# Performance work log

Hardware: AMD Instinct MI355X
Metric: run time of the kernel (lower is better)

## Reference

```python
import jax, jax.numpy as jnp
import numpy as np

EMB_DIM = 256
NUM_EMB = 8192
COMMITMENT = 0.25
DECAY = 0.99
EPSILON = 1e-05


def setup_inputs() -> dict:
    key = jax.random.key(0)
    k1, k2, k3 = jax.random.split(key, 3)
    inputs = jax.random.normal(k1, (32, EMB_DIM, 32, 32), dtype=jnp.float32)
    embed = jax.random.normal(k2, (EMB_DIM, NUM_EMB), dtype=jnp.float32)
    cluster_size = jnp.ones((NUM_EMB,), dtype=jnp.float32)
    ema_embed = jax.random.normal(k3, (EMB_DIM, NUM_EMB), dtype=jnp.float32)
    return {"inputs": inputs, "embed": embed, "cluster_size": cluster_size, "ema_embed": ema_embed}


def reference(inputs, embed, cluster_size, ema_embed):
    # NCHW -> NHWC
    x = jnp.transpose(inputs, (0, 2, 3, 1))  # [B,H,W,D]
    in_shape = x.shape
    flatten = x.reshape(-1, EMB_DIM)  # [N,D]
    N = flatten.shape[0]

    dist = (jnp.sum(flatten ** 2, axis=1, keepdims=True)
            - 2.0 * flatten @ embed
            + jnp.sum(embed ** 2, axis=0, keepdims=True))
    idx = jnp.argmin(dist, axis=1)  # [N]

    # codebook gather
    quantize = embed.T[idx].reshape(in_shape)  # [B,H,W,D]

    # ---- EMA updates (training mode) ----
    counts = jnp.zeros((NUM_EMB,), flatten.dtype).at[idx].add(1.0)  # one-hot col sums
    new_cluster_size = cluster_size * DECAY + (1.0 - DECAY) * counts
    n = jnp.sum(new_cluster_size)
    smoothed = n * ((new_cluster_size + EPSILON) / (n + new_cluster_size * EPSILON))
    dw = jax.ops.segment_sum(flatten, idx, num_segments=NUM_EMB).T  # [D,K] == flatten.T @ onehot
    new_ema_embed = ema_embed * DECAY + (1.0 - DECAY) * dw
    new_embed = new_ema_embed / smoothed[None, :]

    # losses / straight-through
    e_latent_loss = jnp.mean((jax.lax.stop_gradient(quantize) - x) ** 2)
    loss = COMMITMENT * e_latent_loss
    quant_st = x + jax.lax.stop_gradient(quantize - x)

    avg_probs = counts / N
    perplexity = jnp.exp(-jnp.sum(avg_probs * jnp.log(avg_probs + 1e-10)))

    out = jnp.transpose(quant_st, (0, 3, 1, 2))  # back to NCHW
    return (out, loss, perplexity, new_cluster_size, new_embed, new_ema_embed)
```

## Files before the change

### kernel.cpp

```cpp
#include <hip/hip_runtime.h>
#include <math.h>


#define KC 8192
#define DD 256
#define NV 32768

typedef _Float16 f16;
typedef _Float16 f16x8 __attribute__((ext_vector_type(8)));
typedef _Float16 f16x4 __attribute__((ext_vector_type(4)));
typedef float f32x4 __attribute__((ext_vector_type(4)));
typedef unsigned int u32;
typedef unsigned long long u64;

#define DBIAS 4096.0f

__device__ __forceinline__ u32 umin32(u32 a, u32 b) { return a < b ? a : b; }
__device__ __forceinline__ u32 umax32(u32 a, u32 b) { return a > b ? a : b; }

__global__ __launch_bounds__(256, 2) void k_convert_x(
    const float* __restrict__ x, f16* __restrict__ xh, f16* __restrict__ xl,
    float* __restrict__ lossAcc) {
    __shared__ float xs[256][68];
    __shared__ float red[4];
    const int t = threadIdx.x;
    const int n0 = blockIdx.x * 64;
    const int b = n0 >> 10;
    const int h0 = (n0 >> 5) & 31;
    {
        const int p = t >> 7, tt = t & 127;
        const int wq = (tt & 7) * 4, d0 = tt >> 3;
        const float* src = x + (size_t)b * 262144 + (size_t)(h0 + p) * 32 + wq;
        float s2 = 0.f;
        #pragma unroll
        for (int i = 0; i < 16; ++i) {
            int d = d0 + i * 16;
            float4 v = *(const float4*)(src + (size_t)d * 1024);
            *(float4*)&xs[d][p * 32 + wq] = v;
            s2 += v.x * v.x + v.y * v.y + v.z * v.z + v.w * v.w;
        }
        for (int off = 32; off > 0; off >>= 1) s2 += __shfl_xor(s2, off);
        if ((t & 63) == 0) red[t >> 6] = s2;
    }
    __syncthreads();
    if (t == 0) atomicAdd(&lossAcc[1], red[0] + red[1] + red[2] + red[3]);
    {
        const int rr = t & 3, c = t >> 2;
        #pragma unroll
        for (int i = 0; i < 16; ++i) {
            int r = rr + i * 4;
            f16x4 hv, lv;
            #pragma unroll
            for (int q = 0; q < 4; ++q) {
                float v = xs[c * 4 + q][r];
                f16 h = (f16)v;
                float rem = v - (float)h;
                hv[q] = h; lv[q] = (f16)rem;
            }
            *(f16x4*)(xh + (size_t)(n0 + r) * DD + c * 4) = hv;
            *(f16x4*)(xl + (size_t)(n0 + r) * DD + c * 4) = lv;
        }
    }
}

__global__ __launch_bounds__(256, 2) void k_convert_e(
    const float* __restrict__ embed, f16* __restrict__ eh, f16* __restrict__ el,
    float* __restrict__ enorm, float* __restrict__ lossAcc) {
    __shared__ float ps2[8][33];
    __shared__ float psl[8][33];
    const int t = threadIdx.x;
    const int c = t & 31, g = t >> 5;
    const int k = blockIdx.x * 32 + c;
    const int d0 = g * 32;
    f16x8 hv[4], lv[4];
    float s2 = 0.f, sl2 = 0.f;
    #pragma unroll
    for (int i = 0; i < 32; ++i) {
        float v = embed[(size_t)(d0 + i) * KC + k];
        f16 h = (f16)v;
        float rem = v - (float)h;
        f16 lo = (f16)rem;
        hv[i >> 3][i & 7] = h;
        lv[i >> 3][i & 7] = lo;
        s2 += v * v;
        float lf = (float)lo;
        sl2 += lf * lf;
    }
    #pragma unroll
    for (int i = 0; i < 4; ++i) {
        *(f16x8*)(eh + (size_t)k * DD + d0 + i * 8) = hv[i];
        *(f16x8*)(el + (size_t)k * DD + d0 + i * 8) = lv[i];
    }
    ps2[g][c] = s2; psl[g][c] = sl2;
    __syncthreads();
    if (t < 32) {
        float e = 0.f, l = 0.f;
        #pragma unroll
        for (int g2 = 0; g2 < 8; ++g2) { e += ps2[g2][t]; l += psl[g2][t]; }
        enorm[blockIdx.x * 32 + t] = e;
        float me = e, mll = l;
        #pragma unroll
        for (int off = 16; off > 0; off >>= 1) {
            me = fmaxf(me, __shfl_xor(me, off));
            mll = fmaxf(mll, __shfl_xor(mll, off));
        }
        if (t == 0) {
            atomicMax((int*)(lossAcc + 2), __float_as_int(me));
            atomicMax((int*)(lossAcc + 3), __float_as_int(mll));
        }
    }
}


__device__ __forceinline__ void gload16(const void* g, void* l) {
    __builtin_amdgcn_global_load_lds(
        (const __attribute__((address_space(1))) void*)g,
        (__attribute__((address_space(3))) void*)l, 16, 0, 0);
}

#define CFENCE asm volatile("" ::: "memory")
#define BAR()  do { CFENCE; __builtin_amdgcn_s_barrier(); CFENCE; } while (0)
#define WAITV(N) asm volatile("s_waitcnt vmcnt(" #N ")" ::: "memory")
#define WAITL0   asm volatile("s_waitcnt lgkmcnt(0)" ::: "memory")

#define STAGE(KT, NB) do { \
    const f16* _ga = xh + aoff + (KT) * 32; \
    gload16(_ga, ldsAw + (NB) * 16384); \
    gload16(_ga + 16 * DD, ldsAw + (NB) * 16384 + 1024); \
    gload16(eh + boff + (KT) * 32, ldsBw + (NB) * 8192); \
} while (0)

#define PHASE(B, DOSTAGE, SKT, SNB, WN) do { \
    const char* _ab = AsB + (B) * 16384 + abyte; \
    const char* _bb = BsB + (B) * 8192 + bbyte; \
    f16x8 _aav[4], _bbv[4]; \
    _Pragma("unroll") for (int _j = 0; _j < 4; ++_j) _bbv[_j] = *(const f16x8*)(_bb + _j * 1024); \
    _Pragma("unroll") for (int _i = 0; _i < 4; ++_i) _aav[_i] = *(const f16x8*)(_ab + _i * 1024); \
    WAITL0; BAR(); \
    if (DOSTAGE) { STAGE(SKT, SNB); } \
    __builtin_amdgcn_s_setprio(1); \
    _Pragma("unroll") for (int _i = 0; _i < 4; ++_i) \
    _Pragma("unroll") for (int _j = 0; _j < 4; ++_j) \
        acc[_i][_j] = __builtin_amdgcn_mfma_f32_16x16x32_f16(_aav[_i], _bbv[_j], acc[_i][_j], 0, 0, 0); \
    __builtin_amdgcn_s_setprio(0); \
    asm volatile("s_waitcnt vmcnt(" #WN ")" ::: "memory"); BAR(); \
} while (0)

#define PFINAL(B) do { \
    const char* _ab = AsB + (B) * 16384 + abyte; \
    const char* _bb = BsB + (B) * 8192 + bbyte; \
    f16x8 _aav[4], _bbv[4]; \
    _Pragma("unroll") for (int _j = 0; _j < 4; ++_j) _bbv[_j] = *(const f16x8*)(_bb + _j * 1024); \
    _Pragma("unroll") for (int _i = 0; _i < 4; ++_i) _aav[_i] = *(const f16x8*)(_ab + _i * 1024); \
    WAITL0; \
    __builtin_amdgcn_s_setprio(1); \
    _Pragma("unroll") for (int _i = 0; _i < 4; ++_i) \
    _Pragma("unroll") for (int _j = 0; _j < 4; ++_j) \
        acc[_i][_j] = __builtin_amdgcn_mfma_f32_16x16x32_f16(_aav[_i], _bbv[_j], acc[_i][_j], 0, 0, 0); \
    __builtin_amdgcn_s_setprio(0); \
} while (0)

#define DPPSTEP(CTRL) do { \
    u32 _b0 = (u32)__builtin_amdgcn_update_dpp((int)a0v, (int)a0v, CTRL, 0xF, 0xF, false); \
    u32 _b1 = (u32)__builtin_amdgcn_update_dpp((int)a1v, (int)a1v, CTRL, 0xF, 0xF, false); \
    u32 _mx = umax32(a0v, _b0); \
    a0v = umin32(a0v, _b0); \
    a1v = umin32(_mx, umin32(a1v, _b1)); \
} while (0)

__global__ __launch_bounds__(512, 4) void k_gemm_cand(
    const f16* __restrict__ xh, const f16* __restrict__ eh,
    const float* __restrict__ enorm, u64* __restrict__ cand) {
    __shared__ f16 As[3][8192];
    __shared__ f16 Bs[3][4096];
    __shared__ float en_s[128];

    const int t = threadIdx.x;
    const int lane = t & 63, wid = t >> 6;
    const int wr = wid >> 1, wc = wid & 1;
    const int m = lane & 15, q = lane >> 4;

    const int bid = blockIdx.x;
    const int xcd = bid & 7, seq = bid >> 3;
    const int colb = seq >> 4;
    const int rowb = (xcd << 4) | (seq & 15);
    const int BR = rowb * 256;
    const int CBb = colb * 128;

    char* AsB = (char*)&As[0][0];
    char* BsB = (char*)&Bs[0][0];

    if (t < 128) en_s[t] = enorm[CBb + t] + DBIAS;

    const int u8 = lane >> 3, cx = (lane & 7) ^ u8;
    const int stg_row = 2 * u8 + (cx >> 2);
    const int stg_col = (cx & 3) * 8;
    const size_t aoff = (size_t)(BR + wid * 32 + stg_row) * DD + stg_col;
    const size_t boff = (size_t)(CBb + wid * 16 + stg_row) * DD + stg_col;
    char* const ldsAw = AsB + wid * 2048;
    char* const ldsBw = BsB + wid * 1024;

    const int rdsw = (((((m & 1) << 2) | q)) ^ (m >> 1)) * 16;
    const int abyte = wr * 4096 + (m >> 1) * 128 + rdsw;
    const int bbyte = wc * 4096 + (m >> 1) * 128 + rdsw;

    f32x4 acc[4][4];
    #pragma unroll
    for (int i = 0; i < 4; ++i)
        #pragma unroll
        for (int j = 0; j < 4; ++j) acc[i][j] = (f32x4){0.f, 0.f, 0.f, 0.f};

    STAGE(0, 0); STAGE(1, 1);
    WAITV(3); BAR();

    PHASE(0, 1, 2, 2, 3);
    PHASE(1, 1, 3, 0, 3);
    PHASE(2, 1, 4, 1, 3);
    PHASE(0, 1, 5, 2, 3);
    PHASE(1, 1, 6, 0, 3);
    PHASE(2, 1, 7, 1, 3);
    PHASE(0, 0, 0, 0, 0);
    PFINAL(1);

    const int sslab = colb * 2 + wc;
    float enb[4];
    #pragma unroll
    for (int j = 0; j < 4; ++j) enb[j] = en_s[wc * 64 + j * 16 + m];
    #pragma unroll
    for (int i = 0; i < 4; ++i)
    #pragma unroll
    for (int r = 0; r < 4; ++r) {
        u32 kk[4];
        #pragma unroll
        for (int j = 0; j < 4; ++j) {
            float dv = __builtin_fmaf(-2.f, acc[i][j][r], enb[j]);
            kk[j] = (__float_as_uint(dv) & 0xFFFFFFC0u) | (u32)(j * 16 + m);
        }
        u32 s1 = umin32(kk[0], kk[1]), g1 = umax32(kk[0], kk[1]);
        u32 s2 = umin32(kk[2], kk[3]), g2 = umax32(kk[2], kk[3]);
        u32 a0v = umin32(s1, s2);
        u32 a1v = umin32(umax32(s1, s2), umin32(g1, g2));
        DPPSTEP(0x111);
        DPPSTEP(0x112);
        DPPSTEP(0x114);
        DPPSTEP(0x118);
        if (m == 15) {
            int row = BR + wr * 64 + i * 16 + q * 4 + r;
            cand[(size_t)row * 128 + sslab] = ((u64)a1v << 32) | a0v;
        }
    }
}

__global__ __launch_bounds__(256) void k_rescore(
    const u64* __restrict__ cand, const f16* __restrict__ xh, const f16* __restrict__ xl,
    const f16* __restrict__ eh, const f16* __restrict__ el,
    const float* __restrict__ enorm, int* __restrict__ idx, int* __restrict__ cnt,
    float* __restrict__ lossAcc) {
    __shared__ float lred[4];
    const int t = threadIdx.x, l = t & 63, w = t >> 6;
    const int n = blockIdx.x * 4 + w;
    const int l4 = l * 4;

    u64 p0 = cand[(size_t)n * 128 + l];
    u64 p1 = cand[(size_t)n * 128 + 64 + l];
    u32 e0 = (u32)p0, e1 = (u32)(p0 >> 32), e2 = (u32)p1, e3 = (u32)(p1 >> 32);

    u32 mk = umin32(umin32(e0, e1), umin32(e2, e3));
    #pragma unroll
    for (int off = 1; off < 64; off <<= 1)
        mk = umin32(mk, (u32)__shfl_xor((int)mk, off));
    float gminb = __uint_as_float(mk & 0xFFFFFFC0u);

    f16x4 hv = *(const f16x4*)(xh + (size_t)n * DD + l4);
    f16x4 lv = *(const f16x4*)(xl + (size_t)n * DD + l4);
    float xf0 = (float)hv[0] + (float)lv[0];
    float xf1 = (float)hv[1] + (float)lv[1];
    float xf2 = (float)hv[2] + (float)lv[2];
    float xf3 = (float)hv[3] + (float)lv[3];
    float xh2 = (float)hv[0]*(float)hv[0] + (float)hv[1]*(float)hv[1]
              + (float)hv[2]*(float)hv[2] + (float)hv[3]*(float)hv[3];
    float xl2 = (float)lv[0]*(float)lv[0] + (float)lv[1]*(float)lv[1]
              + (float)lv[2]*(float)lv[2] + (float)lv[3]*(float)lv[3];
    #pragma unroll
    for (int off = 1; off < 64; off <<= 1) {
        xh2 += __shfl_xor(xh2, off);
        xl2 += __shfl_xor(xl2, off);
    }
    float maxE2 = lossAcc[2], maxEl2 = lossAcc[3];
    float dlt = 2.f * (sqrtf(xh2) * sqrtf(maxEl2) + sqrtf(xl2) * sqrtf(maxE2));
    float tau = gminb + 2.f * dlt * 1.02f + 0.2f;

    float best = 3.4e38f;
    int bestc = 1 << 30;

#define SLOT(ENT, SBASE) do { \
    float _av = __uint_as_float((ENT) & 0xFFFFFFC0u); \
    u64 _bm = __ballot(_av <= tau); \
    while (_bm) { \
        int _src = __ffsll((unsigned long long)_bm) - 1; _bm &= _bm - 1; \
        u32 _ee = (u32)__shfl((int)(ENT), _src); \
        int _code = ((SBASE) + _src) * 64 + (int)(_ee & 63u); \
        f16x4 _ah = *(const f16x4*)(eh + (size_t)_code * DD + l4); \
        f16x4 _al = *(const f16x4*)(el + (size_t)_code * DD + l4); \
        float _pt = xf0 * ((float)_ah[0] + (float)_al[0]) \
                  + xf1 * ((float)_ah[1] + (float)_al[1]) \
                  + xf2 * ((float)_ah[2] + (float)_al[2]) \
                  + xf3 * ((float)_ah[3] + (float)_al[3]); \
        _pt += __shfl_xor(_pt, 1);  _pt += __shfl_xor(_pt, 2); \
        _pt += __shfl_xor(_pt, 4);  _pt += __shfl_xor(_pt, 8); \
        _pt += __shfl_xor(_pt, 16); _pt += __shfl_xor(_pt, 32); \
        float _d = enorm[_code] - 2.f * _pt; \
        if (_d < best || (_d == best && _code < bestc)) { best = _d; bestc = _code; } \
    } \
} while (0)

    SLOT(e0, 0);
    SLOT(e1, 0);
    SLOT(e2, 64);
    SLOT(e3, 64);
#undef SLOT

    if (l == 0) {
        idx[n] = bestc;
        atomicAdd(&cnt[bestc], 1);
        lred[w] = best;
    }
    __syncthreads();
    if (t == 0) atomicAdd(&lossAcc[0], lred[0] + lred[1] + lred[2] + lred[3]);
}

__global__ void k_stats(const int* __restrict__ cnt, const float* __restrict__ cluster_size,
                        const float* __restrict__ lossAcc,
                        float* __restrict__ out_ncs, float* __restrict__ out_loss,
                        float* __restrict__ out_perp,
                        float* __restrict__ smoothed, int* __restrict__ offsets) {
    __shared__ float rn[256], rp[256];
    __shared__ int rc[256];
    __shared__ int base_s[256];
    int t = threadIdx.x;
    float s_n = 0.f, s_pl = 0.f;
    int s_c = 0;
    float ncs_loc[32];
    #pragma unroll
    for (int i = 0; i < 32; ++i) {
        int k = t * 32 + i;
        int ci = cnt[k];
        float c = (float)ci;
        float ncs = cluster_size[k] * 0.99f + 0.01f * c;
        out_ncs[k] = ncs;
        ncs_loc[i] = ncs;
        s_n += ncs;
        float p = c * (1.0f / 32768.0f);
        s_pl += p * logf(p + 1e-10f);
        s_c += ci;
    }
    rn[t] = s_n; rp[t] = s_pl; rc[t] = s_c;
    for (int off = 128; off > 0; off >>= 1) {
        __syncthreads();
        if (t < off) { rn[t] += rn[t + off]; rp[t] += rp[t + off]; }
    }
    __syncthreads();
    float ntot = rn[0];
    if (t == 0) {
        out_loss[0] = 0.25f * (lossAcc[0] + lossAcc[1]) * (1.0f / 8388608.0f);
        out_perp[0] = expf(-rp[0]);
    }
    #pragma unroll
    for (int i = 0; i < 32; ++i) {
        int k = t * 32 + i;
        float ncs = ncs_loc[i];
        smoothed[k] = ntot * (ncs + 1e-5f) / (ntot + ncs * 1e-5f);
    }
    __syncthreads();
    if (t == 0) {
        int run = 0;
        for (int qq = 0; qq < 256; ++qq) { base_s[qq] = run; run += rc[qq]; }
    }
    __syncthreads();
    int run = base_s[t];
    #pragma unroll
    for (int i = 0; i < 32; ++i) {
        int k = t * 32 + i;
        offsets[k] = run;
        run += cnt[k];
    }
}

__global__ void k_scatter(const int* __restrict__ idx, const int* __restrict__ offsets,
                          int* __restrict__ cursor, int* __restrict__ order) {
    int n = blockIdx.x * 256 + threadIdx.x;
    int k = idx[n];
    int pos = offsets[k] + atomicAdd(&cursor[k], 1);
    order[pos] = n;
}

__global__ __launch_bounds__(512) void k_dw(
    const int* __restrict__ cnt, const int* __restrict__ offsets,
    const int* __restrict__ order, const f16* __restrict__ xh,
    const f16* __restrict__ xl, f16* __restrict__ dwT) {
    __shared__ float part[8][256];
    const int k = blockIdx.x;
    const int t = threadIdx.x, lane = t & 63, w = t >> 6;
    const int c = cnt[k], base = offsets[k];
    const int dq = lane * 4;
    f32x4 sa = (f32x4){0.f, 0.f, 0.f, 0.f};
    f32x4 sb = (f32x4){0.f, 0.f, 0.f, 0.f};
    for (int i = w; i < c; i += 16) {
        const int i2 = i + 8;
        const int n0 = order[base + i];
        const int n1 = (i2 < c) ? order[base + i2] : n0;
        f16x4 h0 = *(const f16x4*)(xh + (size_t)n0 * DD + dq);
        f16x4 l0 = *(const f16x4*)(xl + (size_t)n0 * DD + dq);
        f16x4 h1 = *(const f16x4*)(xh + (size_t)n1 * DD + dq);
        f16x4 l1 = *(const f16x4*)(xl + (size_t)n1 * DD + dq);
        #pragma unroll
        for (int j = 0; j < 4; ++j) sa[j] += (float)h0[j] + (float)l0[j];
        if (i2 < c) {
            #pragma unroll
            for (int j = 0; j < 4; ++j) sb[j] += (float)h1[j] + (float)l1[j];
        }
    }
    #pragma unroll
    for (int j = 0; j < 4; ++j) part[w][dq + j] = sa[j] + sb[j];
    __syncthreads();
    if (t < 256) {
        float s = 0.f;
        #pragma unroll
        for (int w2 = 0; w2 < 8; ++w2) s += part[w2][t];
        dwT[(size_t)k * DD + t] = (f16)s;
    }
}

__global__ void k_update_embed(const f16* __restrict__ dwT, const float* __restrict__ ema_embed,
                               const float* __restrict__ smoothed,
                               float* __restrict__ out_embed, float* __restrict__ out_ema) {
    __shared__ float tile[8][260];
    int bx = blockIdx.x, t = threadIdx.x;
    int d0 = (bx & 31) * 8, k0 = (bx >> 5) * 256;
    {
        f16x8 v = *(const f16x8*)(dwT + (size_t)(k0 + t) * DD + d0);
        #pragma unroll
        for (int j = 0; j < 8; ++j) tile[j][t] = (float)v[j];
    }
    __syncthreads();
    float sm = smoothed[k0 + t];
    #pragma unroll
    for (int dv = 0; dv < 8; ++dv) {
        size_t o = (size_t)(d0 + dv) * KC + k0 + t;
        float dw = tile[dv][t];
        float ne = ema_embed[o] * 0.99f + 0.01f * dw;
        out_ema[o] = ne;
        out_embed[o] = ne / sm;
    }
}

__global__ __launch_bounds__(256, 2) void k_quantize_out(
    const int* __restrict__ idx, const f16* __restrict__ eh, const f16* __restrict__ el,
    float* __restrict__ out) {
    __shared__ float qv[256][68];
    __shared__ int li[64];
    int t = threadIdx.x;
    int n0 = blockIdx.x * 64;
    int b = n0 >> 10, h0 = (n0 >> 5) & 31;
    if (t < 64) li[t] = idx[n0 + t];
    __syncthreads();
    {
        int r = t >> 2, dq4 = (t & 3) * 4;
        const f16* srch = eh + (size_t)li[r] * DD;
        const f16* srcl = el + (size_t)li[r] * DD;
        for (int i = 0; i < 16; ++i) {
            int d = dq4 + i * 16;
            f16x4 hv = *(const f16x4*)(srch + d);
            f16x4 lv = *(const f16x4*)(srcl + d);
            qv[d + 0][r] = (float)hv[0] + (float)lv[0];
            qv[d + 1][r] = (float)hv[1] + (float)lv[1];
            qv[d + 2][r] = (float)hv[2] + (float)lv[2];
            qv[d + 3][r] = (float)hv[3] + (float)lv[3];
        }
    }
    __syncthreads();
    {
        int p = t >> 7, tt = t & 127;
        int wq = (tt & 7) * 4, d0 = tt >> 3;
        float* dst = out + (size_t)b * 262144 + (size_t)(h0 + p) * 32 + wq;
        for (int i = 0; i < 16; ++i) {
            int d = d0 + i * 16;
            float4 v = *(const float4*)&qv[d][p * 32 + wq];
            *(float4*)(dst + (size_t)d * 1024) = v;
        }
    }
}

extern "C" void kernel_launch(void* const* d_in, const int* in_sizes, int n_in,
                              void* d_out, int out_size, void* d_ws, size_t ws_size,
                              hipStream_t stream) {
    (void)in_sizes; (void)n_in; (void)out_size; (void)ws_size;
    const float* x            = (const float*)d_in[0];
    const float* embed        = (const float*)d_in[1];
    const float* cluster_size = (const float*)d_in[2];
    const float* ema_embed    = (const float*)d_in[3];
    float* out = (float*)d_out;
    char* ws = (char*)d_ws;

    f16*   xh       = (f16*)  (ws + 0);
    f16*   xl       = (f16*)  (ws + 16777216);
    f16*   eh       = (f16*)  (ws + 33554432);
    f16*   el       = (f16*)  (ws + 37748736);
    float* enorm    = (float*)(ws + 41943040);
    float* smoothed = (float*)(ws + 41975808);
    int*   idx      = (int*)  (ws + 42008576);
    int*   cnt      = (int*)  (ws + 42139648);
    int*   cursor   = (int*)  (ws + 42172416);
    int*   offsets  = (int*)  (ws + 42205184);
    float* lossAcc  = (float*)(ws + 42237952);
    int*   order    = (int*)  (ws + 42238208);
    f16*   dwT      = (f16*)  (ws + 42500352);

    u64* cand = (u64*)d_out;

    float* out_q    = out;
    float* out_loss = out + 8388608;
    float* out_perp = out + 8388609;
    float* out_ncs  = out + 8388610;
    float* out_emb  = out + 8396802;
    float* out_ema  = out + 10493954;

    hipMemsetAsync(cnt, 0, 65536, stream);
    hipMemsetAsync(lossAcc, 0, 16, stream);

    k_convert_x<<<512, 256, 0, stream>>>(x, xh, xl, lossAcc);
    k_convert_e<<<256, 256, 0, stream>>>(embed, eh, el, enorm, lossAcc);
    k_gemm_cand<<<8192, 512, 0, stream>>>(xh, eh, enorm, cand);
    k_rescore<<<8192, 256, 0, stream>>>(cand, xh, xl, eh, el, enorm, idx, cnt, lossAcc);
    k_stats<<<1, 256, 0, stream>>>(cnt, cluster_size, lossAcc, out_ncs, out_loss, out_perp,
                                   smoothed, offsets);
    k_scatter<<<128, 256, 0, stream>>>(idx, offsets, cursor, order);
    k_dw<<<8192, 512, 0, stream>>>(cnt, offsets, order, xh, xl, dwT);
    k_update_embed<<<1024, 256, 0, stream>>>(dwT, ema_embed, smoothed, out_emb, out_ema);
    k_quantize_out<<<512, 256, 0, stream>>>(idx, eh, el, out_q);
}
```

Baseline: 500.5 us.

## Switch candidate GEMM to double-buffered LDS with syncthreads and higher occupancy

Replaces the triple-buffered GEMM main loop, which used explicit vmcnt and lgkmcnt waits and raw barriers, with a simpler double-buffered loop. Each step stages the next K tile, interleaves per-row A fragment loads with MFMAs, and ends with __syncthreads. The smaller LDS footprint and the raised launch-bounds occupancy hint aim to fit more blocks per CU to hide latency, at the cost of only one tile of prefetch depth and full memory waits at each barrier. The two memsets are merged into one covering the contiguous counter and loss-accumulator region.

Measured after the change: 1.182 ms. 136% more time.

```diff
diff --git a/kernel.cpp b/kernel.cpp
--- a/kernel.cpp
+++ b/kernel.cpp
@@ -118,11 +118,6 @@
         (__attribute__((address_space(3))) void*)l, 16, 0, 0);
 }
 
-#define CFENCE asm volatile("" ::: "memory")
-#define BAR()  do { CFENCE; __builtin_amdgcn_s_barrier(); CFENCE; } while (0)
-#define WAITV(N) asm volatile("s_waitcnt vmcnt(" #N ")" ::: "memory")
-#define WAITL0   asm volatile("s_waitcnt lgkmcnt(0)" ::: "memory")
-
 #define STAGE(KT, NB) do { \
     const f16* _ga = xh + aoff + (KT) * 32; \
     gload16(_ga, ldsAw + (NB) * 16384); \
@@ -130,34 +125,42 @@
     gload16(eh + boff + (KT) * 32, ldsBw + (NB) * 8192); \
 } while (0)
 
-#define PHASE(B, DOSTAGE, SKT, SNB, WN) do { \
+#define BODY(KT, B, NB) do { \
+    STAGE((KT) + 1, NB); \
     const char* _ab = AsB + (B) * 16384 + abyte; \
     const char* _bb = BsB + (B) * 8192 + bbyte; \
-    f16x8 _aav[4], _bbv[4]; \
-    _Pragma("unroll") for (int _j = 0; _j < 4; ++_j) _bbv[_j] = *(const f16x8*)(_bb + _j * 1024); \
-    _Pragma("unroll") for (int _i = 0; _i < 4; ++_i) _aav[_i] = *(const f16x8*)(_ab + _i * 1024); \
-    WAITL0; BAR(); \
-    if (DOSTAGE) { STAGE(SKT, SNB); } \
-    __builtin_amdgcn_s_setprio(1); \
-    _Pragma("unroll") for (int _i = 0; _i < 4; ++_i) \
-    _Pragma("unroll") for (int _j = 0; _j < 4; ++_j) \
-        acc[_i][_j] = __builtin_amdgcn_mfma_f32_16x16x32_f16(_aav[_i], _bbv[_j], acc[_i][_j], 0, 0, 0); \
-    __builtin_amdgcn_s_setprio(0); \
-    asm volatile("s_waitcnt vmcnt(" #WN ")" ::: "memory"); BAR(); \
+    f16x8 _b0 = *(const f16x8*)(_bb); \
+    f16x8 _b1 = *(const f16x8*)(_bb + 1024); \
+    f16x8 _b2 = *(const f16x8*)(_bb + 2048); \
+    f16x8 _b3 = *(const f16x8*)(_bb + 3072); \
+    _Pragma("unroll") for (int _i = 0; _i < 4; ++_i) { \
+        f16x8 _a = *(const f16x8*)(_ab + _i * 1024); \
+        __builtin_amdgcn_s_setprio(1); \
+        acc[_i][0] = __builtin_amdgcn_mfma_f32_16x16x32_f16(_a, _b0, acc[_i][0], 0, 0, 0); \
+        acc[_i][1] = __builtin_amdgcn_mfma_f32_16x16x32_f16(_a, _b1, acc[_i][1], 0, 0, 0); \
+        acc[_i][2] = __builtin_amdgcn_mfma_f32_16x16x32_f16(_a, _b2, acc[_i][2], 0, 0, 0); \
+        acc[_i][3] = __builtin_amdgcn_mfma_f32_16x16x32_f16(_a, _b3, acc[_i][3], 0, 0, 0); \
+        __builtin_amdgcn_s_setprio(0); \
+    } \
+    __syncthreads(); \
 } while (0)
 
-#define PFINAL(B) do { \
+#define FINALT(B) do { \
     const char* _ab = AsB + (B) * 16384 + abyte; \
     const char* _bb = BsB + (B) * 8192 + bbyte; \
-    f16x8 _aav[4], _bbv[4]; \
-    _Pragma("unroll") for (int _j = 0; _j < 4; ++_j) _bbv[_j] = *(const f16x8*)(_bb + _j * 1024); \
-    _Pragma("unroll") for (int _i = 0; _i < 4; ++_i) _aav[_i] = *(const f16x8*)(_ab + _i * 1024); \
-    WAITL0; \
-    __builtin_amdgcn_s_setprio(1); \
-    _Pragma("unroll") for (int _i = 0; _i < 4; ++_i) \
-    _Pragma("unroll") for (int _j = 0; _j < 4; ++_j) \
-        acc[_i][_j] = __builtin_amdgcn_mfma_f32_16x16x32_f16(_aav[_i], _bbv[_j], acc[_i][_j], 0, 0, 0); \
-    __builtin_amdgcn_s_setprio(0); \
+    f16x8 _b0 = *(const f16x8*)(_bb); \
+    f16x8 _b1 = *(const f16x8*)(_bb + 1024); \
+    f16x8 _b2 = *(const f16x8*)(_bb + 2048); \
+    f16x8 _b3 = *(const f16x8*)(_bb + 3072); \
+    _Pragma("unroll") for (int _i = 0; _i < 4; ++_i) { \
+        f16x8 _a = *(const f16x8*)(_ab + _i * 1024); \
+        __builtin_amdgcn_s_setprio(1); \
+        acc[_i][0] = __builtin_amdgcn_mfma_f32_16x16x32_f16(_a, _b0, acc[_i][0], 0, 0, 0); \
+        acc[_i][1] = __builtin_amdgcn_mfma_f32_16x16x32_f16(_a, _b1, acc[_i][1], 0, 0, 0); \
+        acc[_i][2] = __builtin_amdgcn_mfma_f32_16x16x32_f16(_a, _b2, acc[_i][2], 0, 0, 0); \
+        acc[_i][3] = __builtin_amdgcn_mfma_f32_16x16x32_f16(_a, _b3, acc[_i][3], 0, 0, 0); \
+        __builtin_amdgcn_s_setprio(0); \
+    } \
 } while (0)
 
 #define DPPSTEP(CTRL) do { \
@@ -168,11 +171,11 @@
     a1v = umin32(_mx, umin32(a1v, _b1)); \
 } while (0)
 
-__global__ __launch_bounds__(512, 4) void k_gemm_cand(
+__global__ __launch_bounds__(512, 6) void k_gemm_cand(
     const f16* __restrict__ xh, const f16* __restrict__ eh,
     const float* __restrict__ enorm, u64* __restrict__ cand) {
-    __shared__ f16 As[3][8192];
-    __shared__ f16 Bs[3][4096];
+    __shared__ f16 As[2][8192];
+    __shared__ f16 Bs[2][4096];
     __shared__ float en_s[128];
 
     const int t = threadIdx.x;
@@ -210,17 +213,11 @@
         #pragma unroll
         for (int j = 0; j < 4; ++j) acc[i][j] = (f32x4){0.f, 0.f, 0.f, 0.f};
 
-    STAGE(0, 0); STAGE(1, 1);
-    WAITV(3); BAR();
-
-    PHASE(0, 1, 2, 2, 3);
-    PHASE(1, 1, 3, 0, 3);
-    PHASE(2, 1, 4, 1, 3);
-    PHASE(0, 1, 5, 2, 3);
-    PHASE(1, 1, 6, 0, 3);
-    PHASE(2, 1, 7, 1, 3);
-    PHASE(0, 0, 0, 0, 0);
-    PFINAL(1);
+    STAGE(0, 0);
+    __syncthreads();
+    BODY(0, 0, 1); BODY(1, 1, 0); BODY(2, 0, 1); BODY(3, 1, 0);
+    BODY(4, 0, 1); BODY(5, 1, 0); BODY(6, 0, 1);
+    FINALT(1);
 
     const int sslab = colb * 2 + wc;
     float enb[4];
@@ -525,8 +522,7 @@
     float* out_emb  = out + 8396802;
     float* out_ema  = out + 10493954;
 
-    hipMemsetAsync(cnt, 0, 65536, stream);
-    hipMemsetAsync(lossAcc, 0, 16, stream);
+    hipMemsetAsync(cnt, 0, 98320, stream);
 
     k_convert_x<<<512, 256, 0, stream>>>(x, xh, xl, lossAcc);
     k_convert_e<<<256, 256, 0, stream>>>(embed, eh, el, enorm, lossAcc);
```
